# Kernel tuning notes

Hardware: AMD Instinct MI355X
Metric: run time of the kernel (lower is better)

## Reference

```python
import jax, jax.numpy as jnp
import numpy as np
import math

D = 512
H = 512

def setup_inputs() -> dict:
    key = jax.random.key(0)
    k1, k2, k3, k4 = jax.random.split(key, 4)
    x = jax.random.normal(k1, (64, 1024, D), dtype=jnp.float32)
    h0 = jax.random.normal(k2, (64, H), dtype=jnp.float32)
    Wx = jax.random.normal(k3, (D, 4 * H), dtype=jnp.float32) / math.sqrt(D)
    Wh = jax.random.normal(k4, (H, 4 * H), dtype=jnp.float32) / math.sqrt(H)
    b = jnp.zeros((4 * H,), dtype=jnp.float32)
    return {"x": x, "h0": h0, "Wx": Wx, "Wh": Wh, "b": b}

def reference(x, h0, Wx, Wh, b):
    # x: (N,T,D), h0: (N,H). Precompute input projections for all steps at once.
    Hd = h0.shape[-1]
    xW = jnp.einsum('ntd,df->ntf', x, Wx) + b  # (N,T,4H)

    def step(carry, xw_t):
        h, c = carry
        A = xw_t + h @ Wh  # (N,4H)
        i = jax.nn.sigmoid(A[:, :Hd])
        f = jax.nn.sigmoid(A[:, Hd:2 * Hd])
        o = jax.nn.sigmoid(A[:, 2 * Hd:3 * Hd])
        g = jnp.tanh(A[:, 3 * Hd:])
        c_next = f * c + i * g
        h_next = o * jnp.tanh(c_next)
        return (h_next, c_next), h_next

    c0 = jnp.zeros_like(h0)
    # scan over time axis: move T to leading dim
    _, hs = jax.lax.scan(step, (h0, c0), jnp.swapaxes(xW, 0, 1))  # (T,N,H)
    return jnp.swapaxes(hs, 0, 1)  # (N,T,H)
```

## Files before the change

kernel.cpp:

```cpp
#include <hip/hip_runtime.h>
#include <hip/hip_bf16.h>
#include <math.h>


#define TT 1024
#define HH 512
#define FH 2048
#define KK 1024
#define NN 64

typedef __attribute__((ext_vector_type(8))) short bf16x8;
typedef __attribute__((ext_vector_type(4))) float f32x4;
typedef __attribute__((ext_vector_type(4))) int int4v;

__device__ __forceinline__ unsigned short f2bf(float f) {
    return __builtin_bit_cast(unsigned short, __float2bfloat16(f));
}

__global__ __launch_bounds__(256)
void prep_wt(const float* __restrict__ Wx, const float* __restrict__ Wh,
             unsigned short* __restrict__ Wt)
{
    __shared__ float tile[64][65];
    const int c0  = blockIdx.x * 64;
    const int k0  = blockIdx.y * 64;
    const int tid = threadIdx.x;

    #pragma unroll
    for (int it = 0; it < 16; ++it) {
        int idx = it * 256 + tid;
        int kk = idx >> 6, cc = idx & 63;
        int k = k0 + kk;
        float w = (k < 512) ? Wx[(size_t)k * FH + c0 + cc]
                            : Wh[(size_t)(k - 512) * FH + c0 + cc];
        tile[kk][cc] = w;
    }
    __syncthreads();

    #pragma unroll
    for (int it = 0; it < 8; ++it) {
        int idx = it * 256 + tid;
        int cc = idx >> 5, kp = idx & 31;
        unsigned int lo = f2bf(tile[kp * 2][cc]);
        unsigned int hi = f2bf(tile[kp * 2 + 1][cc]);
        *(unsigned int*)(Wt + (size_t)(c0 + cc) * KK + k0 + kp * 2) =
            lo | (hi << 16);
    }
}

__global__ __launch_bounds__(256)
void lstm_init(const float* __restrict__ h0,
               unsigned short* __restrict__ hb,
               unsigned int* __restrict__ flg)
{
    int id = blockIdx.x * 256 + threadIdx.x;
    if (id < 256 * 16) {
        unsigned int* p = flg + id;
        unsigned int z = 0u;
        asm volatile("global_store_dword %0, %1, off sc0 sc1" :: "v"(p), "v"(z) : "memory");
    }
    if (id < NN * HH) {
        unsigned int hv = (unsigned int)f2bf(h0[id]);
        unsigned short* hp = hb + id;
        asm volatile("global_store_short %0, %1, off sc0 sc1" :: "v"(hp), "v"(hv) : "memory");
    }
}

__global__ __launch_bounds__(512, 2)
void lstm_persist(const float* __restrict__ x,
                  const unsigned short* __restrict__ Wt,
                  const float* __restrict__ bias,
                  float* __restrict__ out,
                  unsigned short* __restrict__ hb,
                  unsigned int* __restrict__ flg)
{
    __shared__ __align__(16) unsigned short Ap[16 * 1024];
    __shared__ float part[8][16][16];
    __shared__ float As[16][33];

    const int tid  = threadIdx.x;
    const int wv   = tid >> 6;
    const int lane = tid & 63;
    const int l15  = lane & 15;
    const int kh   = lane >> 4;

    const int rg = blockIdx.x >> 6;
    const int jg = blockIdx.x & 63;
    const int j0 = jg * 8;
    const int rowbase = rg * 16;

    const int ct = wv & 1;
    const int kq = wv >> 1;

    const int lc   = ct * 16 + l15;
    const int gate = lc >> 3;
    const int jj   = lc & 7;
    const int gcol = gate * HH + j0 + jj;

    const unsigned short* wtp = Wt + (size_t)gcol * KK + kh * 8;
    bf16x8 bx[4], bh[4];
    #pragma unroll
    for (int ks = 0; ks < 4; ++ks) {
        bx[ks] = *(const bf16x8*)(wtp + kq * 128 + ks * 32);
        bh[ks] = *(const bf16x8*)(wtp + 512 + kq * 128 + ks * 32);
    }

    const int arow = l15;
    const int rsw  = (arow & 7) << 3;
    const unsigned short* apr = Ap + arow * 1024;

    const int srow = tid >> 5;
    const int scol = tid & 31;
    const int rws  = (srow & 7) << 3;
    const float* xrow_ptr = x + (size_t)(rowbase + srow) * TT * 512 + scol * 16;

    const int grow_l = (tid < 128) ? (tid >> 3) : 0;
    const int q      = tid & 7;
    const int grow   = rowbase + grow_l;
    const int gj     = j0 + q;
    float bi = 0.f, bf_ = 0.f, bo = 0.f, bg = 0.f;
    if (tid < 128) {
        bi  = bias[gj];
        bf_ = bias[HH + gj];
        bo  = bias[2 * HH + gj];
        bg  = bias[3 * HH + gj];
    }
    float c_reg = 0.f;
    float* outp = out + (size_t)grow * TT * HH + gj;
    unsigned short* hdst0 = hb + (size_t)grow * HH + gj;

    unsigned int* myflag = flg + (size_t)blockIdx.x * 16;
    const unsigned int* pollp = flg + (size_t)(rg * 64 + lane) * 16;

    float4 xpf[4];
    #pragma unroll
    for (int i = 0; i < 4; ++i)
        xpf[i] = *(const float4*)(xrow_ptr + i * 4);

    for (int t = 0; t < TT; ++t) {
        const int cur = t & 1;
        const int nxt = cur ^ 1;

        {
            unsigned int pk[8];
            #pragma unroll
            for (int i = 0; i < 4; ++i) {
                pk[2 * i]     = (unsigned int)f2bf(xpf[i].x) | ((unsigned int)f2bf(xpf[i].y) << 16);
                pk[2 * i + 1] = (unsigned int)f2bf(xpf[i].z) | ((unsigned int)f2bf(xpf[i].w) << 16);
            }
            int k0u = scol * 16;
            *(int4v*)(Ap + srow * 1024 + (k0u ^ rws))       = *(int4v*)&pk[0];
            *(int4v*)(Ap + srow * 1024 + ((k0u + 8) ^ rws)) = *(int4v*)&pk[4];
        }
        __syncthreads();

        f32x4 acc = {0.f, 0.f, 0.f, 0.f};
        #pragma unroll
        for (int ks = 0; ks < 4; ++ks) {
            bf16x8 a = *(const bf16x8*)(apr + ((kq * 128 + ks * 32 + kh * 8) ^ rsw));
            acc = __builtin_amdgcn_mfma_f32_16x16x32_bf16(a, bx[ks], acc, 0, 0, 0);
        }

        if (t > 0) {
            unsigned int v;
            do {
                asm volatile("global_load_dword %0, %1, off sc0 sc1\n\t"
                             "s_waitcnt vmcnt(0)"
                             : "=v"(v) : "v"(pollp) : "memory");
            } while (!__all(v >= (unsigned int)t));
        }

        if (t + 1 < TT) {
            #pragma unroll
            for (int i = 0; i < 4; ++i)
                xpf[i] = *(const float4*)(xrow_ptr + (size_t)(t + 1) * 512 + i * 4);
        }

        {
            const unsigned short* hsrc = hb + (size_t)cur * NN * HH
                                       + (size_t)(rowbase + srow) * HH + scol * 16;
            int4v h0v, h1v;
            asm volatile("global_load_dwordx4 %0, %1, off sc0 sc1" : "=v"(h0v) : "v"(hsrc));
            asm volatile("global_load_dwordx4 %0, %1, off sc0 sc1" : "=v"(h1v) : "v"(hsrc + 8));
            asm volatile("s_waitcnt vmcnt(0)" ::: "memory");
            int k0u = 512 + scol * 16;
            *(int4v*)(Ap + srow * 1024 + (k0u ^ rws))       = h0v;
            *(int4v*)(Ap + srow * 1024 + ((k0u + 8) ^ rws)) = h1v;
        }
        __syncthreads();

        #pragma unroll
        for (int ks = 0; ks < 4; ++ks) {
            bf16x8 a = *(const bf16x8*)(apr + ((512 + kq * 128 + ks * 32 + kh * 8) ^ rsw));
            acc = __builtin_amdgcn_mfma_f32_16x16x32_bf16(a, bh[ks], acc, 0, 0, 0);
        }
        #pragma unroll
        for (int rr = 0; rr < 4; ++rr)
            part[wv][kh * 4 + rr][l15] = acc[rr];
        __syncthreads();

        {
            int row = tid >> 5;
            int lc2 = tid & 31;
            int ct2 = lc2 >> 4;
            int cc  = lc2 & 15;
            As[row][lc2] = part[ct2][row][cc] + part[2 + ct2][row][cc]
                         + part[4 + ct2][row][cc] + part[6 + ct2][row][cc];
        }
        __syncthreads();

        if (tid < 128) {
            float Ai = As[grow_l][q]      + bi;
            float Af = As[grow_l][8 + q]  + bf_;
            float Ao = As[grow_l][16 + q] + bo;
            float Ag = As[grow_l][24 + q] + bg;
            float ig = 1.f / (1.f + __expf(-Ai));
            float fg = 1.f / (1.f + __expf(-Af));
            float og = 1.f / (1.f + __expf(-Ao));
            float gg = tanhf(Ag);
            c_reg = fg * c_reg + ig * gg;
            float hn = og * tanhf(c_reg);
            outp[(size_t)t * HH] = hn;
            unsigned int hv = (unsigned int)f2bf(hn);
            unsigned short* hdst = hdst0 + (size_t)nxt * NN * HH;
            asm volatile("global_store_short %0, %1, off sc0 sc1" :: "v"(hdst), "v"(hv) : "memory");
        }

        if (t + 1 < TT) {
            asm volatile("s_waitcnt vmcnt(0)" ::: "memory");
            __syncthreads();
            if (tid == 0) {
                unsigned int target = (unsigned int)(t + 1);
                asm volatile("global_store_dword %0, %1, off sc0 sc1"
                             :: "v"(myflag), "v"(target) : "memory");
            }
        }
    }
}

extern "C" void kernel_launch(void* const* d_in, const int* in_sizes, int n_in,
                              void* d_out, int out_size, void* d_ws, size_t ws_size,
                              hipStream_t stream)
{
    const float* x  = (const float*)d_in[0];
    const float* h0 = (const float*)d_in[1];
    const float* Wx = (const float*)d_in[2];
    const float* Wh = (const float*)d_in[3];
    const float* b  = (const float*)d_in[4];
    float* out = (float*)d_out;

    char* ws = (char*)d_ws;
    unsigned short* Wt  = (unsigned short*)ws;
    unsigned short* hb  = (unsigned short*)(ws + (size_t)4 * 1024 * 1024);
    unsigned int*   flg = (unsigned int*)(ws + (size_t)4 * 1024 * 1024 + 131072);

    prep_wt<<<dim3(32, 16), 256, 0, stream>>>(Wx, Wh, Wt);
    lstm_init<<<128, 256, 0, stream>>>(h0, hb, flg);
    lstm_persist<<<256, 512, 0, stream>>>(x, Wt, b, out, hb, flg);
}
```

Baseline: 3.280 ms.

## Load MFMA operands straight into registers and cut per-step block barriers

Removes the shared-memory staging of x and h tiles. Each lane now loads its MFMA A-operand fragments directly from global memory into registers. The partial-sum reduction is folded into the gate computation using a double-buffered part array, which cuts the per-step __syncthreads from four to one. Flags are split per half-block: two writer threads each publish after their own h stores, and pollers check only the flags they depend on. tanh is replaced by exp-based formulas. This shortens the serial critical path of each recurrent step, at the cost of more global load traffic per lane and subtle memory-ordering assumptions in the split flags.

```diff
diff --git a/kernel.cpp b/kernel.cpp
--- a/kernel.cpp
+++ b/kernel.cpp
@@ -66,7 +66,7 @@
     }
 }
 
-__global__ __launch_bounds__(512, 2)
+__global__ __launch_bounds__(512)
 void lstm_persist(const float* __restrict__ x,
                   const unsigned short* __restrict__ Wt,
                   const float* __restrict__ bias,
@@ -74,9 +74,7 @@
                   unsigned short* __restrict__ hb,
                   unsigned int* __restrict__ flg)
 {
-    __shared__ __align__(16) unsigned short Ap[16 * 1024];
-    __shared__ float part[8][16][16];
-    __shared__ float As[16][33];
+    __shared__ float part[2][8][16][20];
 
     const int tid  = threadIdx.x;
     const int wv   = tid >> 6;
@@ -105,18 +103,12 @@
         bh[ks] = *(const bf16x8*)(wtp + 512 + kq * 128 + ks * 32);
     }
 
-    const int arow = l15;
-    const int rsw  = (arow & 7) << 3;
-    const unsigned short* apr = Ap + arow * 1024;
-
-    const int srow = tid >> 5;
-    const int scol = tid & 31;
-    const int rws  = (srow & 7) << 3;
-    const float* xrow_ptr = x + (size_t)(rowbase + srow) * TT * 512 + scol * 16;
-
-    const int grow_l = (tid < 128) ? (tid >> 3) : 0;
+    const float* xbase = x + (size_t)(rowbase + l15) * TT * 512 + kq * 128 + kh * 8;
+    const unsigned short* hlane = hb + (size_t)(rowbase + l15) * HH + kq * 128 + kh * 8;
+
+    const int grow_l = tid >> 3;
     const int q      = tid & 7;
-    const int grow   = rowbase + grow_l;
+    const int grow   = rowbase + (grow_l & 15);
     const int gj     = j0 + q;
     float bi = 0.f, bf_ = 0.f, bo = 0.f, bg = 0.f;
     if (tid < 128) {
@@ -129,110 +121,130 @@
     float* outp = out + (size_t)grow * TT * HH + gj;
     unsigned short* hdst0 = hb + (size_t)grow * HH + gj;
 
-    unsigned int* myflag = flg + (size_t)blockIdx.x * 16;
-    const unsigned int* pollp = flg + (size_t)(rg * 64 + lane) * 16;
-
-    float4 xpf[4];
-    #pragma unroll
-    for (int i = 0; i < 4; ++i)
-        xpf[i] = *(const float4*)(xrow_ptr + i * 4);
+    const unsigned int* pollp = flg
+        + (size_t)(rg * 64 + kq * 16 + (lane & 15)) * 16
+        + ((lane >> 4) & 1) * 8;
+
+    unsigned int* myflag = flg + (size_t)blockIdx.x * 16 + ((tid == 64) ? 8 : 0);
+
+    float4 xpf[8];
+    #pragma unroll
+    for (int ks = 0; ks < 4; ++ks) {
+        xpf[2 * ks]     = *(const float4*)(xbase + ks * 32);
+        xpf[2 * ks + 1] = *(const float4*)(xbase + ks * 32 + 4);
+    }
+    bf16x8 xf[4];
+    #pragma unroll
+    for (int ks = 0; ks < 4; ++ks) {
+        bf16x8 a;
+        a[0] = (short)f2bf(xpf[2 * ks].x);     a[1] = (short)f2bf(xpf[2 * ks].y);
+        a[2] = (short)f2bf(xpf[2 * ks].z);     a[3] = (short)f2bf(xpf[2 * ks].w);
+        a[4] = (short)f2bf(xpf[2 * ks + 1].x); a[5] = (short)f2bf(xpf[2 * ks + 1].y);
+        a[6] = (short)f2bf(xpf[2 * ks + 1].z); a[7] = (short)f2bf(xpf[2 * ks + 1].w);
+        xf[ks] = a;
+    }
 
     for (int t = 0; t < TT; ++t) {
+        const int pb  = t & 1;
         const int cur = t & 1;
         const int nxt = cur ^ 1;
 
+        if (t > 0) {
+            const unsigned int tgt = (unsigned int)t;
+            unsigned int v = 0xFFFFFFFFu;
+            do {
+                if (lane < 32) {
+                    asm volatile("global_load_dword %0, %1, off sc0 sc1\n\t"
+                                 "s_waitcnt vmcnt(0)"
+                                 : "=v"(v) : "v"(pollp) : "memory");
+                }
+            } while (!__all(v >= tgt));
+        }
+
+        int4v hr[4];
         {
-            unsigned int pk[8];
-            #pragma unroll
-            for (int i = 0; i < 4; ++i) {
-                pk[2 * i]     = (unsigned int)f2bf(xpf[i].x) | ((unsigned int)f2bf(xpf[i].y) << 16);
-                pk[2 * i + 1] = (unsigned int)f2bf(xpf[i].z) | ((unsigned int)f2bf(xpf[i].w) << 16);
-            }
-            int k0u = scol * 16;
-            *(int4v*)(Ap + srow * 1024 + (k0u ^ rws))       = *(int4v*)&pk[0];
-            *(int4v*)(Ap + srow * 1024 + ((k0u + 8) ^ rws)) = *(int4v*)&pk[4];
-        }
-        __syncthreads();
+            const unsigned short* hp = hlane + (size_t)cur * NN * HH;
+            #pragma unroll
+            for (int ks = 0; ks < 4; ++ks) {
+                asm volatile("global_load_dwordx4 %0, %1, off sc0 sc1"
+                             : "=v"(hr[ks]) : "v"(hp + ks * 32));
+            }
+        }
+
+        if (t + 1 < TT) {
+            const float* xp = xbase + (size_t)(t + 1) * 512;
+            #pragma unroll
+            for (int ks = 0; ks < 4; ++ks) {
+                xpf[2 * ks]     = *(const float4*)(xp + ks * 32);
+                xpf[2 * ks + 1] = *(const float4*)(xp + ks * 32 + 4);
+            }
+        }
 
         f32x4 acc = {0.f, 0.f, 0.f, 0.f};
         #pragma unroll
-        for (int ks = 0; ks < 4; ++ks) {
-            bf16x8 a = *(const bf16x8*)(apr + ((kq * 128 + ks * 32 + kh * 8) ^ rsw));
-            acc = __builtin_amdgcn_mfma_f32_16x16x32_bf16(a, bx[ks], acc, 0, 0, 0);
-        }
-
-        if (t > 0) {
-            unsigned int v;
-            do {
-                asm volatile("global_load_dword %0, %1, off sc0 sc1\n\t"
-                             "s_waitcnt vmcnt(0)"
-                             : "=v"(v) : "v"(pollp) : "memory");
-            } while (!__all(v >= (unsigned int)t));
-        }
+        for (int ks = 0; ks < 4; ++ks)
+            acc = __builtin_amdgcn_mfma_f32_16x16x32_bf16(xf[ks], bx[ks], acc, 0, 0, 0);
 
         if (t + 1 < TT) {
-            #pragma unroll
-            for (int i = 0; i < 4; ++i)
-                xpf[i] = *(const float4*)(xrow_ptr + (size_t)(t + 1) * 512 + i * 4);
-        }
-
-        {
-            const unsigned short* hsrc = hb + (size_t)cur * NN * HH
-                                       + (size_t)(rowbase + srow) * HH + scol * 16;
-            int4v h0v, h1v;
-            asm volatile("global_load_dwordx4 %0, %1, off sc0 sc1" : "=v"(h0v) : "v"(hsrc));
-            asm volatile("global_load_dwordx4 %0, %1, off sc0 sc1" : "=v"(h1v) : "v"(hsrc + 8));
+            asm volatile("s_waitcnt vmcnt(8)" ::: "memory");
+        } else {
             asm volatile("s_waitcnt vmcnt(0)" ::: "memory");
-            int k0u = 512 + scol * 16;
-            *(int4v*)(Ap + srow * 1024 + (k0u ^ rws))       = h0v;
-            *(int4v*)(Ap + srow * 1024 + ((k0u + 8) ^ rws)) = h1v;
-        }
-        __syncthreads();
+        }
+        __builtin_amdgcn_sched_barrier(0);
 
         #pragma unroll
-        for (int ks = 0; ks < 4; ++ks) {
-            bf16x8 a = *(const bf16x8*)(apr + ((512 + kq * 128 + ks * 32 + kh * 8) ^ rsw));
-            acc = __builtin_amdgcn_mfma_f32_16x16x32_bf16(a, bh[ks], acc, 0, 0, 0);
-        }
+        for (int ks = 0; ks < 4; ++ks)
+            acc = __builtin_amdgcn_mfma_f32_16x16x32_bf16(
+                __builtin_bit_cast(bf16x8, hr[ks]), bh[ks], acc, 0, 0, 0);
+
         #pragma unroll
         for (int rr = 0; rr < 4; ++rr)
-            part[wv][kh * 4 + rr][l15] = acc[rr];
+            part[pb][wv][kh * 4 + rr][l15] = acc[rr];
+
         __syncthreads();
 
-        {
-            int row = tid >> 5;
-            int lc2 = tid & 31;
-            int ct2 = lc2 >> 4;
-            int cc  = lc2 & 15;
-            As[row][lc2] = part[ct2][row][cc] + part[2 + ct2][row][cc]
-                         + part[4 + ct2][row][cc] + part[6 + ct2][row][cc];
-        }
-        __syncthreads();
-
         if (tid < 128) {
-            float Ai = As[grow_l][q]      + bi;
-            float Af = As[grow_l][8 + q]  + bf_;
-            float Ao = As[grow_l][16 + q] + bo;
-            float Ag = As[grow_l][24 + q] + bg;
+            float Ai = bi, Af = bf_, Ao = bo, Ag = bg;
+            #pragma unroll
+            for (int k2 = 0; k2 < 4; ++k2) {
+                Ai += part[pb][2 * k2][grow_l][q];
+                Af += part[pb][2 * k2][grow_l][q + 8];
+                Ao += part[pb][2 * k2 + 1][grow_l][q];
+                Ag += part[pb][2 * k2 + 1][grow_l][q + 8];
+            }
             float ig = 1.f / (1.f + __expf(-Ai));
             float fg = 1.f / (1.f + __expf(-Af));
             float og = 1.f / (1.f + __expf(-Ao));
-            float gg = tanhf(Ag);
+            float eg = __expf(2.f * Ag);
+            float gg = 1.f - 2.f / (eg + 1.f);
             c_reg = fg * c_reg + ig * gg;
-            float hn = og * tanhf(c_reg);
-            outp[(size_t)t * HH] = hn;
+            float ec = __expf(2.f * c_reg);
+            float tc = 1.f - 2.f / (ec + 1.f);
+            float hn = og * tc;
+
             unsigned int hv = (unsigned int)f2bf(hn);
             unsigned short* hdst = hdst0 + (size_t)nxt * NN * HH;
-            asm volatile("global_store_short %0, %1, off sc0 sc1" :: "v"(hdst), "v"(hv) : "memory");
+            asm volatile("global_store_short %0, %1, off sc0 sc1"
+                         :: "v"(hdst), "v"(hv) : "memory");
+            asm volatile("s_waitcnt vmcnt(0)" ::: "memory");
+            if (t + 1 < TT && (tid == 0 || tid == 64)) {
+                unsigned int tgt = (unsigned int)(t + 1);
+                asm volatile("global_store_dword %0, %1, off sc0 sc1"
+                             :: "v"(myflag), "v"(tgt) : "memory");
+            }
+            outp[(size_t)t * HH] = hn;
         }
 
         if (t + 1 < TT) {
             asm volatile("s_waitcnt vmcnt(0)" ::: "memory");
-            __syncthreads();
-            if (tid == 0) {
-                unsigned int target = (unsigned int)(t + 1);
-                asm volatile("global_store_dword %0, %1, off sc0 sc1"
-                             :: "v"(myflag), "v"(target) : "memory");
+            #pragma unroll
+            for (int ks = 0; ks < 4; ++ks) {
+                bf16x8 a;
+                a[0] = (short)f2bf(xpf[2 * ks].x);     a[1] = (short)f2bf(xpf[2 * ks].y);
+                a[2] = (short)f2bf(xpf[2 * ks].z);     a[3] = (short)f2bf(xpf[2 * ks].w);
+                a[4] = (short)f2bf(xpf[2 * ks + 1].x); a[5] = (short)f2bf(xpf[2 * ks + 1].y);
+                a[6] = (short)f2bf(xpf[2 * ks + 1].z); a[7] = (short)f2bf(xpf[2 * ks + 1].w);
+                xf[ks] = a;
             }
         }
     }
```

Measured after the change: 5.185 ms. +58.1%, slower.
